# Optimization experiments

Measured on AMD Instinct MI355X. Metric: run time of the kernel, lower is better.

Reference implementation:

```python
import jax, jax.numpy as jnp
import numpy as np

NUM_NODES = 200000   # visited nodes in the temporal-KG subgraph
D = 64               # n_dims_in == n_dims_out
Q = 128              # number of query subgraphs (edges[:,0])
E = 1024             # edges per query group (equal-size groups)
NE = Q * E
RATIO = 0.0          # ratio_update
NEG_SLOPE = 0.01     # LeakyReLU default


def setup_inputs() -> dict:
    key = jax.random.key(0)
    ks = jax.random.split(key, 10)
    qid = jnp.repeat(jnp.arange(Q, dtype=jnp.int32), E)          # edges[:,0]
    src = jax.random.randint(ks[0], (NE,), 0, NUM_NODES, dtype=jnp.int32)
    dst = jax.random.randint(ks[1], (NE,), 0, NUM_NODES, dtype=jnp.int32)
    zeros = jnp.zeros((NE,), dtype=jnp.int32)
    # cols: 0=query idx, 1..5 unused metadata, 6=src (-2), 7=dst (-1)
    edges = jnp.stack([qid, zeros, zeros, zeros, zeros, zeros, src, dst], axis=1)
    std_g3 = np.sqrt(2.0 / (4 * D)).astype(np.float32)
    return {
        "node_score": jax.random.uniform(ks[2], (NUM_NODES,), dtype=jnp.float32),
        "node_repr": jax.random.normal(ks[3], (NUM_NODES, D), dtype=jnp.float32),
        "rel_emb": jax.random.normal(ks[4], (NE, D), dtype=jnp.float32),
        "query_src_ts_emb": jax.random.normal(ks[5], (Q, D), dtype=jnp.float32),
        "query_rel_emb": jax.random.normal(ks[6], (Q, D), dtype=jnp.float32),
        "Wq": jax.random.normal(ks[7], (4 * D, 4 * D), dtype=jnp.float32) * std_g3,
        "Wk": jax.random.normal(ks[8], (4 * D, 4 * D), dtype=jnp.float32) * std_g3,
        "W_lin": jax.random.normal(ks[9], (D, D), dtype=jnp.float32) * np.sqrt(2.0 / (2 * D)).astype(np.float32),
        "b_lin": jnp.zeros((D,), dtype=jnp.float32),
        "edges": edges,
        "max_edges": 128,
    }


def _segment_softmax(logits, seg, num_segments):
    # numerically stable softmax within segments (per src node)
    m = jax.ops.segment_max(logits, seg, num_segments=num_segments)
    ex = jnp.exp(logits - m[seg])
    s = jax.ops.segment_sum(ex, seg, num_segments=num_segments)
    return ex / s[seg]


def reference(node_score, node_repr, rel_emb, query_src_ts_emb, query_rel_emb,
              Wq, Wk, W_lin, b_lin, edges, max_edges):
    q = edges[:, 0]
    src = edges[:, 6]   # edges[:, -2]
    dst = edges[:, 7]   # edges[:, -1] (same as col 7 used for sparse rows)
    qs = query_src_ts_emb[q]   # [NE, D]
    qr = query_rel_emb[q]      # [NE, D]
    # G3 bilinear attention: sum(Q(left) * K(right), -1)
    left = jnp.concatenate([node_repr[src], rel_emb, qs, qr], axis=-1)   # [NE, 4D]
    right = jnp.concatenate([node_repr[dst], rel_emb, qs, qr], axis=-1)  # [NE, 4D]
    logits = jnp.sum((left @ Wq.T) * (right @ Wk.T), axis=-1)            # [NE]
    # segment softmax over src nodes, score propagation
    soft = _segment_softmax(logits, src, NUM_NODES)
    src_score = node_score[src]
    target_score = soft * src_score
    # top-k per query group (equal-size groups -> vectorized top_k)
    _, idx = jax.lax.top_k(target_score.reshape(Q, E), max_edges)        # [Q, k]
    flat = (jnp.arange(Q, dtype=idx.dtype)[:, None] * E + idx).reshape(-1)
    p_soft = soft[flat]
    p_src = src[flat]
    p_dst = dst[flat]
    p_src_score = src_score[flat]
    # sparse scatter: updated_node_score[dst] += softmax * src_score
    updated_node_score = jax.ops.segment_sum(p_soft * p_src_score, p_dst, num_segments=NUM_NODES)
    # representation update: rows src aggregate dst reprs weighted by softmax;
    # untouched nodes keep identity, touched src nodes keep ratio_update of self
    agg = jax.ops.segment_sum((1.0 - RATIO) * p_soft[:, None] * node_repr[p_dst],
                              p_src, num_segments=NUM_NODES)             # [N, D]
    is_src = jnp.zeros((NUM_NODES,), bool).at[p_src].set(True)
    diag = jnp.where(is_src, RATIO, 1.0)
    updated_repr = agg + diag[:, None] * node_repr
    # bypass_forward: LeakyReLU(Linear(.))
    out_repr = jax.nn.leaky_relu(updated_repr @ W_lin + b_lin, NEG_SLOPE)
    return updated_node_score, out_repr
```

## Files before the change

### kernel.cpp

```cpp
#include <hip/hip_runtime.h>

#define NNODES 200000
#define NQ     128
#define EPQ    1024
#define NE     (NQ*EPQ)
#define TOPK   128
#define NSEL   (NQ*TOPK)

__device__ __forceinline__ unsigned fkey(float f) {
  unsigned u = __float_as_uint(f);
  return (u & 0x80000000u) ? ~u : (u | 0x80000000u);
}
__device__ __forceinline__ float fdecode(unsigned k) {
  unsigned u = (k & 0x80000000u) ? (k ^ 0x80000000u) : ~k;
  return __uint_as_float(u);
}
__device__ __forceinline__ void fmarow(float* a, float x, const float4 n0, const float4 n1) {
  a[0] = fmaf(x, n0.x, a[0]); a[1] = fmaf(x, n0.y, a[1]);
  a[2] = fmaf(x, n0.z, a[2]); a[3] = fmaf(x, n0.w, a[3]);
  a[4] = fmaf(x, n1.x, a[4]); a[5] = fmaf(x, n1.y, a[5]);
  a[6] = fmaf(x, n1.z, a[6]); a[7] = fmaf(x, n1.w, a[7]);
}

typedef const __attribute__((address_space(1))) void* gas_ptr;
typedef __attribute__((address_space(3))) void* las_ptr;
__device__ __forceinline__ void gload16(const void* g, void* l) {
  __builtin_amdgcn_global_load_lds((gas_ptr)g, (las_ptr)l, 16, 0, 0);
}

__device__ __forceinline__ int nperm(int k) {
  const int q = k >> 2, p = k & 3;
  return (q & 1) * 64 + (q >> 1) * 4 + p;
}

__global__ __launch_bounds__(256) void k_init(unsigned* __restrict__ segmax,
                                              float* __restrict__ segsum,
                                              int* __restrict__ flag,
                                              float* __restrict__ outs) {
  const int i = blockIdx.x * 256 + threadIdx.x;
  if (i < NNODES) { segmax[i] = 0u; segsum[i] = 0.f; flag[i] = 0; outs[i] = 0.f; }
}

__global__ __launch_bounds__(256) void k_nmat(const float* __restrict__ Wq,
                                              const float* __restrict__ Wk,
                                              float* __restrict__ Nm) {
  __shared__ float ph[128];
  const int j = blockIdx.x;
  const int k = threadIdx.x & 127;
  const int ih = threadIdx.x >> 7;
  const int i0 = ih * 128;
  float a0 = 0.f, a1 = 0.f, a2 = 0.f, a3 = 0.f;
  for (int i = i0; i < i0 + 128; i += 4) {
    a0 = fmaf(Wq[(i + 0) * 256 + j], Wk[(i + 0) * 256 + k], a0);
    a1 = fmaf(Wq[(i + 1) * 256 + j], Wk[(i + 1) * 256 + k], a1);
    a2 = fmaf(Wq[(i + 2) * 256 + j], Wk[(i + 2) * 256 + k], a2);
    a3 = fmaf(Wq[(i + 3) * 256 + j], Wk[(i + 3) * 256 + k], a3);
  }
  const float p = (a0 + a1) + (a2 + a3);
  if (ih == 0) ph[k] = p;
  __syncthreads();
  if (ih == 1) Nm[j * 128 + nperm(k)] = ph[k] + p;
}

__global__ __launch_bounds__(256) void k_query(const float* __restrict__ Wq,
                                               const float* __restrict__ Wk,
                                               const float* __restrict__ qs_emb,
                                               const float* __restrict__ qr_emb,
                                               float* __restrict__ alpha,
                                               float* __restrict__ beta,
                                               float* __restrict__ cv) {
  __shared__ float sq[128];
  __shared__ float u[256], v[256];
  const int q = blockIdx.x, t = threadIdx.x;
  if (t < 64) sq[t] = qs_emb[q * 64 + t];
  else if (t < 128) sq[t] = qr_emb[q * 64 + (t - 64)];
  __syncthreads();
  {
    const float4* wq4 = (const float4*)(Wq + t * 256 + 128);
    const float4* wk4 = (const float4*)(Wk + t * 256 + 128);
    const float4* sq4 = (const float4*)sq;
    float uu = 0.f, vv = 0.f;
#pragma unroll 8
    for (int j = 0; j < 32; ++j) {
      const float4 a = wq4[j], b = wk4[j], s = sq4[j];
      uu = fmaf(a.x, s.x, fmaf(a.y, s.y, fmaf(a.z, s.z, fmaf(a.w, s.w, uu))));
      vv = fmaf(b.x, s.x, fmaf(b.y, s.y, fmaf(b.z, s.z, fmaf(b.w, s.w, vv))));
    }
    u[t] = uu; v[t] = vv;
  }
  __syncthreads();
  if (t < 128) {
    float a0 = 0.f, a1 = 0.f, a2 = 0.f, a3 = 0.f;
    for (int i = 0; i < 256; i += 4) {
      a0 = fmaf(Wq[(i + 0) * 256 + t], v[i + 0], a0);
      a1 = fmaf(Wq[(i + 1) * 256 + t], v[i + 1], a1);
      a2 = fmaf(Wq[(i + 2) * 256 + t], v[i + 2], a2);
      a3 = fmaf(Wq[(i + 3) * 256 + t], v[i + 3], a3);
    }
    alpha[q * 128 + t] = (a0 + a1) + (a2 + a3);
  } else {
    const int k = t - 128;
    float b0 = 0.f, b1 = 0.f, b2 = 0.f, b3 = 0.f;
    for (int i = 0; i < 256; i += 4) {
      b0 = fmaf(u[i + 0], Wk[(i + 0) * 256 + k], b0);
      b1 = fmaf(u[i + 1], Wk[(i + 1) * 256 + k], b1);
      b2 = fmaf(u[i + 2], Wk[(i + 2) * 256 + k], b2);
      b3 = fmaf(u[i + 3], Wk[(i + 3) * 256 + k], b3);
    }
    beta[q * 128 + k] = (b0 + b1) + (b2 + b3);
  }
  __syncthreads();
  if (t < 64) {
    float c = u[t] * v[t] + u[t + 64] * v[t + 64] + u[t + 128] * v[t + 128] + u[t + 192] * v[t + 192];
    c += __shfl_xor(c, 32, 64);
    c += __shfl_xor(c, 16, 64);
    c += __shfl_xor(c, 8, 64);
    c += __shfl_xor(c, 4, 64);
    c += __shfl_xor(c, 2, 64);
    c += __shfl_xor(c, 1, 64);
    if (t == 0) cv[q] = c;
  }
}

__global__ __launch_bounds__(512, 1) void k_logits(
    const float* __restrict__ repr, const float* __restrict__ rel,
    const int* __restrict__ edges, const float* __restrict__ Nm,
    const float* __restrict__ alpha, const float* __restrict__ beta,
    const float* __restrict__ cv, float* __restrict__ logits) {
  __shared__ float Nl[128 * 128];
  __shared__ float Xe[256 * 64];
  __shared__ float sA[128], sB[128];
  __shared__ int sSrc[256], sDst[256];
  const int t = threadIdx.x;
  const int e0 = blockIdx.x * 256;
  const int q = e0 >> 10;

  {
    const char* g = (const char*)Nm + (size_t)t * 16;
    char* l = (char*)Nl + (size_t)t * 16;
#pragma unroll
    for (int r = 0; r < 8; ++r) gload16(g + r * 8192, l + r * 8192);
  }

  if (t < 256) {
    sSrc[t] = edges[(size_t)(e0 + t) * 8 + 6];
    sDst[t] = edges[(size_t)(e0 + t) * 8 + 7];
  } else if (t < 384) {
    sA[t - 256] = alpha[q * 128 + (t - 256)];
  } else {
    sB[t - 384] = beta[q * 128 + (t - 384)];
  }

  const int elr = t >> 4, c = t & 15;
  const int swzst = (elr >> 3) & 3;
#pragma unroll
  for (int r = 0; r < 8; ++r) {
    const int el = r * 32 + elr;
    const int src = edges[(size_t)(e0 + el) * 8 + 6];
    const int cg = c ^ swzst;
    gload16((const char*)repr + ((size_t)src * 64 + cg * 4) * 4,
            (char*)Xe + ((size_t)el * 64 + c * 4) * 4);
  }
  __syncthreads();

  const int kg = t & 15, eg = t >> 4;
  const int k0 = kg * 8, eb = eg * 8;
  const int kf = kg * 4;
  const int swz = eg & 3;
  float acc[8][8];
#pragma unroll
  for (int i = 0; i < 8; ++i)
#pragma unroll
    for (int m = 0; m < 8; ++m) acc[i][m] = 0.f;

#pragma unroll 2
  for (int J = 0; J < 16; ++J) {
    const float* __restrict__ Nr = Nl + (4 * J) * 128;
    float4 n0[4], n1[4];
#pragma unroll
    for (int jj = 0; jj < 4; ++jj) {
      n0[jj] = *(const float4*)(Nr + jj * 128 + kf);
      n1[jj] = *(const float4*)(Nr + jj * 128 + 64 + kf);
    }
    const int ch = (J ^ swz) * 4;
    float4 xv[8];
#pragma unroll
    for (int i = 0; i < 8; ++i)
      xv[i] = *(const float4*)(Xe + (eb + i) * 64 + ch);
#pragma unroll
    for (int jj = 0; jj < 4; ++jj) {
#pragma unroll
      for (int i = 0; i < 8; ++i) {
        const float xs = jj == 0 ? xv[i].x : jj == 1 ? xv[i].y : jj == 2 ? xv[i].z : xv[i].w;
        fmarow(acc[i], xs, n0[jj], n1[jj]);
      }
    }
  }
  __syncthreads();

#pragma unroll
  for (int r = 0; r < 8; ++r) {
    const int el = r * 32 + elr;
    const int cg = c ^ swzst;
    gload16((const char*)rel + ((size_t)(e0 + el) * 64 + cg * 4) * 4,
            (char*)Xe + ((size_t)el * 64 + c * 4) * 4);
  }
  __syncthreads();

#pragma unroll 2
  for (int J = 0; J < 16; ++J) {
    const float* __restrict__ Nr = Nl + (64 + 4 * J) * 128;
    float4 n0[4], n1[4];
#pragma unroll
    for (int jj = 0; jj < 4; ++jj) {
      n0[jj] = *(const float4*)(Nr + jj * 128 + kf);
      n1[jj] = *(const float4*)(Nr + jj * 128 + 64 + kf);
    }
    const int ch = (J ^ swz) * 4;
    float4 xv[8];
#pragma unroll
    for (int i = 0; i < 8; ++i)
      xv[i] = *(const float4*)(Xe + (eb + i) * 64 + ch);
#pragma unroll
    for (int jj = 0; jj < 4; ++jj) {
#pragma unroll
      for (int i = 0; i < 8; ++i) {
        const float xs = jj == 0 ? xv[i].x : jj == 1 ? xv[i].y : jj == 2 ? xv[i].z : xv[i].w;
        fmarow(acc[i], xs, n0[jj], n1[jj]);
      }
    }
  }

  float aA[8], aB[8];
#pragma unroll
  for (int m = 0; m < 8; ++m) { aA[m] = sA[k0 + m]; aB[m] = sB[k0 + m]; }

  float part[8];
#pragma unroll
  for (int i = 0; i < 8; ++i) {
    const int el = eb + i;
    const int e = e0 + el;
    const float* xp;
    const float* yp;
    if (k0 < 64) {
      xp = repr + (size_t)sSrc[el] * 64 + k0;
      yp = repr + (size_t)sDst[el] * 64 + k0;
    } else {
      xp = rel + (size_t)e * 64 + (k0 - 64);
      yp = xp;
    }
    const float4 x0 = *(const float4*)xp;
    const float4 x1 = *(const float4*)(xp + 4);
    const float4 y0 = *(const float4*)yp;
    const float4 y1 = *(const float4*)(yp + 4);
    const float xs[8] = {x0.x, x0.y, x0.z, x0.w, x1.x, x1.y, x1.z, x1.w};
    const float ys[8] = {y0.x, y0.y, y0.z, y0.w, y1.x, y1.y, y1.z, y1.w};
    float p = 0.f;
#pragma unroll
    for (int m = 0; m < 8; ++m)
      p += (acc[i][m] + aB[m]) * ys[m] + aA[m] * xs[m];
    part[i] = p;
  }
#pragma unroll
  for (int i = 0; i < 8; ++i) {
    float p = part[i];
    p += __shfl_xor(p, 8, 64);
    p += __shfl_xor(p, 4, 64);
    p += __shfl_xor(p, 2, 64);
    p += __shfl_xor(p, 1, 64);
    part[i] = p;
  }
  if (kg == 0) {
    const float cq = cv[q];
    float4 o0 = {part[0] + cq, part[1] + cq, part[2] + cq, part[3] + cq};
    float4 o1 = {part[4] + cq, part[5] + cq, part[6] + cq, part[7] + cq};
    *(float4*)(logits + e0 + eb) = o0;
    *(float4*)(logits + e0 + eb + 4) = o1;
  }
}

__global__ __launch_bounds__(256) void k_segmax(const float* __restrict__ logits,
                                                const int* __restrict__ edges,
                                                unsigned* __restrict__ segmax) {
  const int e = blockIdx.x * 256 + threadIdx.x;
  const int src = edges[(size_t)e * 8 + 6];
  atomicMax(&segmax[src], fkey(logits[e]));
}

__global__ __launch_bounds__(256) void k_exsum(float* __restrict__ logits,
                                               const int* __restrict__ edges,
                                               const unsigned* __restrict__ segmax,
                                               float* __restrict__ segsum) {
  const int e = blockIdx.x * 256 + threadIdx.x;
  const int src = edges[(size_t)e * 8 + 6];
  const float m = fdecode(segmax[src]);
  const float ex = expf(logits[e] - m);
  logits[e] = ex;
  atomicAdd(&segsum[src], ex);
}

__global__ __launch_bounds__(256) void k_topk(const float* __restrict__ ex,
                                              const float* __restrict__ segsum,
                                              const int* __restrict__ edges,
                                              const float* __restrict__ node_score,
                                              int* __restrict__ sel,
                                              int* __restrict__ flag,
                                              float* __restrict__ out_score,
                                              float* agg) {
  __shared__ unsigned keys[1024];
  __shared__ int hist[256];
  __shared__ int selEl[128];
  __shared__ int eqIdx[32];
  __shared__ int sB0, sRank, sCnt, sEq;
  const int q = blockIdx.x, t = threadIdx.x;
  for (int i = t; i < 1024; i += 256) {
    const int e = q * 1024 + i;
    const int src = edges[(size_t)e * 8 + 6];
    const float ts = (ex[e] / segsum[src]) * node_score[src];
    keys[i] = fkey(ts);
  }
  unsigned prefix = 0, pmask = 0;
  int rank = 128;
  __syncthreads();
#pragma unroll
  for (int pass = 0; pass < 4; ++pass) {
    const int shift = 24 - 8 * pass;
    hist[t] = 0;
    __syncthreads();
    for (int i = t; i < 1024; i += 256) {
      const unsigned k = keys[i];
      if ((k & pmask) == prefix) atomicAdd(&hist[(k >> shift) & 255], 1);
    }
    __syncthreads();
    if (t < 64) {
      const int h0 = hist[4 * t], h1 = hist[4 * t + 1], h2 = hist[4 * t + 2], h3 = hist[4 * t + 3];
      const int s4 = h0 + h1 + h2 + h3;
      int S = s4;
      for (int d = 1; d < 64; d <<= 1) {
        const int o = __shfl_down(S, d, 64);
        if (t + d < 64) S += o;
      }
      const int Snext = S - s4;
      if (S >= rank && Snext < rank) {
        int r = rank - Snext;
        int b;
        if (r <= h3) b = 3;
        else if (r <= h3 + h2) { b = 2; r -= h3; }
        else if (r <= h3 + h2 + h1) { b = 1; r -= h3 + h2; }
        else { b = 0; r -= h3 + h2 + h1; }
        sB0 = 4 * t + b; sRank = r;
      }
    }
    __syncthreads();
    prefix |= ((unsigned)sB0) << shift;
    pmask |= 0xFFu << shift;
    rank = sRank;
    __syncthreads();
  }
  const unsigned thr = prefix;
  if (t == 0) { sCnt = 0; sEq = 0; }
  __syncthreads();
  for (int i = t; i < 1024; i += 256) {
    const unsigned k = keys[i];
    if (k > thr) { const int s = atomicAdd(&sCnt, 1); selEl[s] = i; }
    else if (k == thr) { const int j = atomicAdd(&sEq, 1); if (j < 32) eqIdx[j] = i; }
  }
  __syncthreads();
  if (t == 0) {
    int n = sEq; if (n > 32) n = 32;
    for (int a = 1; a < n; ++a) {
      const int v2 = eqIdx[a]; int b = a - 1;
      while (b >= 0 && eqIdx[b] > v2) { eqIdx[b + 1] = eqIdx[b]; --b; }
      eqIdx[b + 1] = v2;
    }
    for (int r2 = 0; r2 < rank; ++r2) selEl[sCnt + r2] = eqIdx[r2];
  }
  __syncthreads();
  if (t < 128) {
    const int el = selEl[t];
    const int e = q * 1024 + el;
    sel[q * 128 + t] = e;
    const int src = edges[(size_t)e * 8 + 6];
    const int dst = edges[(size_t)e * 8 + 7];
    const float soft = ex[e] / segsum[src];
    atomicAdd(&out_score[dst], soft * node_score[src]);
    flag[src] = 1;
  }
  __syncthreads();
  for (int i = t; i < 128 * 64; i += 256) {
    const int s = i >> 6, d = i & 63;
    const int e = q * 1024 + selEl[s];
    const int src = edges[(size_t)e * 8 + 6];
    agg[(size_t)src * 64 + d] = 0.f;
  }
}

__global__ __launch_bounds__(256) void k_scatter(const int* __restrict__ sel,
                                                 const int* __restrict__ edges,
                                                 const float* __restrict__ ex,
                                                 const float* __restrict__ segsum,
                                                 const float* __restrict__ repr,
                                                 float* agg) {
  const int i = blockIdx.x * 4 + (threadIdx.x >> 6);
  const int d = threadIdx.x & 63;
  const int e = sel[i];
  const int src = edges[(size_t)e * 8 + 6];
  const int dst = edges[(size_t)e * 8 + 7];
  const float soft = ex[e] / segsum[src];
  atomicAdd(&agg[(size_t)src * 64 + d], soft * repr[(size_t)dst * 64 + d]);
}

#define FN 192
__global__ __launch_bounds__(192) void k_final(const float* __restrict__ repr,
                                               const float* agg,
                                               const int* __restrict__ flag,
                                               const float* __restrict__ Wl,
                                               const float* __restrict__ bl,
                                               float* outr) {
  __shared__ float Ut[64][FN];
  __shared__ float W[64][64];
  __shared__ float bs[64];
  const int t = threadIdx.x;
  const int n0blk = blockIdx.x * FN;
  for (int i = t; i < 4096; i += FN) W[i >> 6][i & 63] = Wl[i];
  if (t < 64) bs[t] = bl[t];
  {
    const int n = n0blk + t;
    const bool ok = n < NNODES;
    const float* rowp = repr;
    if (ok) rowp = (flag[n] ? agg : repr) + (size_t)n * 64;
#pragma unroll
    for (int i = 0; i < 16; ++i) {
      float4 v4 = ok ? ((const float4*)rowp)[i] : float4{0.f, 0.f, 0.f, 0.f};
      const int c = i * 4;
      Ut[c + 0][t] = v4.x; Ut[c + 1][t] = v4.y; Ut[c + 2][t] = v4.z; Ut[c + 3][t] = v4.w;
    }
  }
  __syncthreads();
  const int dg = t & 7, ng = t >> 3;
  const int d0 = dg * 8, nb = ng * 8;
  float acc[8][8];
#pragma unroll
  for (int i = 0; i < 8; ++i)
#pragma unroll
    for (int m = 0; m < 8; ++m) acc[i][m] = 0.f;
#pragma unroll 2
  for (int c = 0; c < 64; ++c) {
    const float4 w0 = *(const float4*)&W[c][d0];
    const float4 w1 = *(const float4*)&W[c][d0 + 4];
    const float4 u0 = *(const float4*)&Ut[c][nb];
    const float4 u1 = *(const float4*)&Ut[c][nb + 4];
    fmarow(acc[0], u0.x, w0, w1);
    fmarow(acc[1], u0.y, w0, w1);
    fmarow(acc[2], u0.z, w0, w1);
    fmarow(acc[3], u0.w, w0, w1);
    fmarow(acc[4], u1.x, w0, w1);
    fmarow(acc[5], u1.y, w0, w1);
    fmarow(acc[6], u1.z, w0, w1);
    fmarow(acc[7], u1.w, w0, w1);
  }
  float bb[8];
#pragma unroll
  for (int m = 0; m < 8; ++m) bb[m] = bs[d0 + m];
#pragma unroll
  for (int i = 0; i < 8; ++i) {
    const int n = n0blk + nb + i;
    if (n < NNODES) {
      float o[8];
#pragma unroll
      for (int m = 0; m < 8; ++m) {
        float v = acc[i][m] + bb[m];
        o[m] = v > 0.f ? v : 0.01f * v;
      }
      float4 o0 = {o[0], o[1], o[2], o[3]};
      float4 o1 = {o[4], o[5], o[6], o[7]};
      *(float4*)(outr + (size_t)n * 64 + d0) = o0;
      *(float4*)(outr + (size_t)n * 64 + d0 + 4) = o1;
    }
  }
}

extern "C" void kernel_launch(void* const* d_in, const int* in_sizes, int n_in,
                              void* d_out, int out_size, void* d_ws, size_t ws_size,
                              hipStream_t stream) {
  const float* node_score = (const float*)d_in[0];
  const float* node_repr  = (const float*)d_in[1];
  const float* rel_emb    = (const float*)d_in[2];
  const float* qs_emb     = (const float*)d_in[3];
  const float* qr_emb     = (const float*)d_in[4];
  const float* Wq         = (const float*)d_in[5];
  const float* Wk         = (const float*)d_in[6];
  const float* Wl         = (const float*)d_in[7];
  const float* bl         = (const float*)d_in[8];
  const int*   edges      = (const int*)d_in[9];

  float* out_score = (float*)d_out;
  float* out_repr  = out_score + NNODES;

  float* ws = (float*)d_ws;
  size_t o = 0;
  float* Nm      = ws + o; o += 128 * 128;
  float* alpha   = ws + o; o += NQ * 128;
  float* beta    = ws + o; o += NQ * 128;
  float* cv      = ws + o; o += NQ;
  float* exl     = ws + o; o += NE;
  unsigned* segmax = (unsigned*)(ws + o); o += NNODES;
  float* segsum  = ws + o; o += NNODES;
  int* sel       = (int*)(ws + o); o += NSEL;
  int* flag      = (int*)(ws + o); o += NNODES;

  k_init<<<(NNODES + 255) / 256, 256, 0, stream>>>(segmax, segsum, flag, out_score);
  k_nmat<<<128, 256, 0, stream>>>(Wq, Wk, Nm);
  k_query<<<NQ, 256, 0, stream>>>(Wq, Wk, qs_emb, qr_emb, alpha, beta, cv);
  k_logits<<<NE / 256, 512, 0, stream>>>(node_repr, rel_emb, edges, Nm, alpha, beta, cv, exl);
  k_segmax<<<NE / 256, 256, 0, stream>>>(exl, edges, segmax);
  k_exsum<<<NE / 256, 256, 0, stream>>>(exl, edges, segmax, segsum);
  k_topk<<<NQ, 256, 0, stream>>>(exl, segsum, edges, node_score, sel, flag, out_score, out_repr);
  k_scatter<<<NSEL / 4, 256, 0, stream>>>(sel, edges, exl, segsum, node_repr, out_repr);
  k_final<<<(NNODES + FN - 1) / FN, FN, 0, stream>>>(node_repr, out_repr, flag, Wl, bl, out_repr);
}
```

Baseline: 175.6 us.

## Double-buffer edge feature chunks and double edges per block in logits kernel

The logits kernel now processes 512 edges per block instead of 256, with each thread accumulating 16 edges. The 128-wide input features (gathered repr then rel) are streamed in 16-column chunks through a two-slot LDS buffer, so the next chunk's async load overlaps the current chunk's FMAs. This halves how often the 64KB N matrix is loaded per edge and hides gather latency. In exchange the grid shrinks to 256 blocks, there are more syncs, and register pressure roughly doubles with 128 accumulators per thread, which risks spills.

```diff
diff --git a/kernel.cpp b/kernel.cpp
--- a/kernel.cpp
+++ b/kernel.cpp
@@ -128,11 +128,11 @@
     const float* __restrict__ alpha, const float* __restrict__ beta,
     const float* __restrict__ cv, float* __restrict__ logits) {
   __shared__ float Nl[128 * 128];
-  __shared__ float Xe[256 * 64];
+  __shared__ float Xp[2][512 * 16];
   __shared__ float sA[128], sB[128];
-  __shared__ int sSrc[256], sDst[256];
+  __shared__ int sSrc[512], sDst[512];
   const int t = threadIdx.x;
-  const int e0 = blockIdx.x * 256;
+  const int e0 = blockIdx.x * 512;
   const int q = e0 >> 10;
 
   {
@@ -142,102 +142,89 @@
     for (int r = 0; r < 8; ++r) gload16(g + r * 8192, l + r * 8192);
   }
 
-  if (t < 256) {
-    sSrc[t] = edges[(size_t)(e0 + t) * 8 + 6];
-    sDst[t] = edges[(size_t)(e0 + t) * 8 + 7];
-  } else if (t < 384) {
-    sA[t - 256] = alpha[q * 128 + (t - 256)];
-  } else {
-    sB[t - 384] = beta[q * 128 + (t - 384)];
-  }
-
-  const int elr = t >> 4, c = t & 15;
-  const int swzst = (elr >> 3) & 3;
-#pragma unroll
-  for (int r = 0; r < 8; ++r) {
-    const int el = r * 32 + elr;
+  {
+    const size_t e = (size_t)(e0 + t);
+    sSrc[t] = edges[e * 8 + 6];
+    sDst[t] = edges[e * 8 + 7];
+    if (t < 128) sA[t] = alpha[q * 128 + t];
+    else if (t < 256) sB[t - 128] = beta[q * 128 + (t - 128)];
+  }
+
+  const int elr = t >> 2, cc = t & 3;
+#pragma unroll
+  for (int r = 0; r < 4; ++r) {
+    const int el = r * 128 + elr;
     const int src = edges[(size_t)(e0 + el) * 8 + 6];
-    const int cg = c ^ swzst;
+    const int cg = cc ^ ((el >> 4) & 3);
     gload16((const char*)repr + ((size_t)src * 64 + cg * 4) * 4,
-            (char*)Xe + ((size_t)el * 64 + c * 4) * 4);
+            (char*)&Xp[0][0] + (size_t)r * 8192 + (size_t)t * 16);
   }
   __syncthreads();
 
   const int kg = t & 15, eg = t >> 4;
-  const int k0 = kg * 8, eb = eg * 8;
+  const int k0 = kg * 8, eb = eg * 16;
   const int kf = kg * 4;
   const int swz = eg & 3;
-  float acc[8][8];
-#pragma unroll
-  for (int i = 0; i < 8; ++i)
+  float acc[16][8];
+#pragma unroll
+  for (int i = 0; i < 16; ++i)
 #pragma unroll
     for (int m = 0; m < 8; ++m) acc[i][m] = 0.f;
 
-#pragma unroll 2
-  for (int J = 0; J < 16; ++J) {
-    const float* __restrict__ Nr = Nl + (4 * J) * 128;
-    float4 n0[4], n1[4];
-#pragma unroll
-    for (int jj = 0; jj < 4; ++jj) {
-      n0[jj] = *(const float4*)(Nr + jj * 128 + kf);
-      n1[jj] = *(const float4*)(Nr + jj * 128 + 64 + kf);
-    }
-    const int ch = (J ^ swz) * 4;
-    float4 xv[8];
-#pragma unroll
-    for (int i = 0; i < 8; ++i)
-      xv[i] = *(const float4*)(Xe + (eb + i) * 64 + ch);
-#pragma unroll
-    for (int jj = 0; jj < 4; ++jj) {
-#pragma unroll
-      for (int i = 0; i < 8; ++i) {
-        const float xs = jj == 0 ? xv[i].x : jj == 1 ? xv[i].y : jj == 2 ? xv[i].z : xv[i].w;
-        fmarow(acc[i], xs, n0[jj], n1[jj]);
+  for (int p = 0; p < 8; ++p) {
+    if (p < 7) {
+      const int pn = p + 1;
+      char* ldst = (char*)&Xp[pn & 1][0] + (size_t)t * 16;
+      if (pn < 4) {
+#pragma unroll
+        for (int r = 0; r < 4; ++r) {
+          const int el = r * 128 + elr;
+          const int src = sSrc[el];
+          const int cg = cc ^ ((el >> 4) & 3);
+          gload16((const char*)repr + ((size_t)src * 64 + pn * 16 + cg * 4) * 4,
+                  ldst + r * 8192);
+        }
+      } else {
+#pragma unroll
+        for (int r = 0; r < 4; ++r) {
+          const int el = r * 128 + elr;
+          const int cg = cc ^ ((el >> 4) & 3);
+          gload16((const char*)rel + ((size_t)(e0 + el) * 64 + (pn - 4) * 16 + cg * 4) * 4,
+                  ldst + r * 8192);
+        }
       }
     }
-  }
-  __syncthreads();
-
-#pragma unroll
-  for (int r = 0; r < 8; ++r) {
-    const int el = r * 32 + elr;
-    const int cg = c ^ swzst;
-    gload16((const char*)rel + ((size_t)(e0 + el) * 64 + cg * 4) * 4,
-            (char*)Xe + ((size_t)el * 64 + c * 4) * 4);
-  }
-  __syncthreads();
-
-#pragma unroll 2
-  for (int J = 0; J < 16; ++J) {
-    const float* __restrict__ Nr = Nl + (64 + 4 * J) * 128;
-    float4 n0[4], n1[4];
-#pragma unroll
-    for (int jj = 0; jj < 4; ++jj) {
-      n0[jj] = *(const float4*)(Nr + jj * 128 + kf);
-      n1[jj] = *(const float4*)(Nr + jj * 128 + 64 + kf);
-    }
-    const int ch = (J ^ swz) * 4;
-    float4 xv[8];
-#pragma unroll
-    for (int i = 0; i < 8; ++i)
-      xv[i] = *(const float4*)(Xe + (eb + i) * 64 + ch);
-#pragma unroll
-    for (int jj = 0; jj < 4; ++jj) {
-#pragma unroll
-      for (int i = 0; i < 8; ++i) {
-        const float xs = jj == 0 ? xv[i].x : jj == 1 ? xv[i].y : jj == 2 ? xv[i].z : xv[i].w;
-        fmarow(acc[i], xs, n0[jj], n1[jj]);
+    const float* __restrict__ Xb = &Xp[p & 1][0];
+#pragma unroll
+    for (int J = 0; J < 4; ++J) {
+      const int jb = p * 16 + J * 4;
+      float4 n0[4], n1[4];
+#pragma unroll
+      for (int jj = 0; jj < 4; ++jj) {
+        const float* Nr = Nl + (jb + jj) * 128;
+        n0[jj] = *(const float4*)(Nr + kf);
+        n1[jj] = *(const float4*)(Nr + 64 + kf);
       }
-    }
+      const int ch = (J ^ swz) * 4;
+#pragma unroll
+      for (int i = 0; i < 16; ++i) {
+        const float4 xv = *(const float4*)(Xb + (eb + i) * 16 + ch);
+        fmarow(acc[i], xv.x, n0[0], n1[0]);
+        fmarow(acc[i], xv.y, n0[1], n1[1]);
+        fmarow(acc[i], xv.z, n0[2], n1[2]);
+        fmarow(acc[i], xv.w, n0[3], n1[3]);
+      }
+    }
+    __syncthreads();
   }
 
   float aA[8], aB[8];
 #pragma unroll
   for (int m = 0; m < 8; ++m) { aA[m] = sA[k0 + m]; aB[m] = sB[k0 + m]; }
 
-  float part[8];
-#pragma unroll
-  for (int i = 0; i < 8; ++i) {
+  float part[16];
+#pragma unroll
+  for (int i = 0; i < 16; ++i) {
     const int el = eb + i;
     const int e = e0 + el;
     const float* xp;
@@ -262,7 +249,7 @@
     part[i] = p;
   }
 #pragma unroll
-  for (int i = 0; i < 8; ++i) {
+  for (int i = 0; i < 16; ++i) {
     float p = part[i];
     p += __shfl_xor(p, 8, 64);
     p += __shfl_xor(p, 4, 64);
@@ -272,10 +259,12 @@
   }
   if (kg == 0) {
     const float cq = cv[q];
-    float4 o0 = {part[0] + cq, part[1] + cq, part[2] + cq, part[3] + cq};
-    float4 o1 = {part[4] + cq, part[5] + cq, part[6] + cq, part[7] + cq};
-    *(float4*)(logits + e0 + eb) = o0;
-    *(float4*)(logits + e0 + eb + 4) = o1;
+#pragma unroll
+    for (int w = 0; w < 4; ++w) {
+      float4 o = {part[w * 4 + 0] + cq, part[w * 4 + 1] + cq,
+                  part[w * 4 + 2] + cq, part[w * 4 + 3] + cq};
+      *(float4*)(logits + e0 + eb + w * 4) = o;
+    }
   }
 }
 
@@ -512,7 +501,7 @@
   k_init<<<(NNODES + 255) / 256, 256, 0, stream>>>(segmax, segsum, flag, out_score);
   k_nmat<<<128, 256, 0, stream>>>(Wq, Wk, Nm);
   k_query<<<NQ, 256, 0, stream>>>(Wq, Wk, qs_emb, qr_emb, alpha, beta, cv);
-  k_logits<<<NE / 256, 512, 0, stream>>>(node_repr, rel_emb, edges, Nm, alpha, beta, cv, exl);
+  k_logits<<<NE / 512, 512, 0, stream>>>(node_repr, rel_emb, edges, Nm, alpha, beta, cv, exl);
   k_segmax<<<NE / 256, 256, 0, stream>>>(exl, edges, segmax);
   k_exsum<<<NE / 256, 256, 0, stream>>>(exl, edges, segmax, segsum);
   k_topk<<<NQ, 256, 0, stream>>>(exl, segsum, edges, node_score, sel, flag, out_score, out_repr);
```

New measurement: 252.7 us. 43.9% more time.

## Merge setup kernels, fuse segment-max into logits, compact edge src/dst columns

Applied to the files above, without the earlier changes.

Folds the init, N-matrix and per-query kernels into one launch that dispatches on block index. The segment-max atomics move into the logits kernel's epilogue, and the logits kernel writes compact src/dst arrays that later kernels read instead of the strided 8-int edge rows. The top-k kernel goes from 256 to 512 threads per block. This removes three launches and one pass over logits and edges, at the cost of extra workspace and more atomic traffic in the logits epilogue.

```diff
diff --git a/kernel.cpp b/kernel.cpp
--- a/kernel.cpp
+++ b/kernel.cpp
@@ -33,45 +33,43 @@
   return (q & 1) * 64 + (q >> 1) * 4 + p;
 }
 
-__global__ __launch_bounds__(256) void k_init(unsigned* __restrict__ segmax,
-                                              float* __restrict__ segsum,
-                                              int* __restrict__ flag,
-                                              float* __restrict__ outs) {
-  const int i = blockIdx.x * 256 + threadIdx.x;
-  if (i < NNODES) { segmax[i] = 0u; segsum[i] = 0.f; flag[i] = 0; outs[i] = 0.f; }
-}
-
-__global__ __launch_bounds__(256) void k_nmat(const float* __restrict__ Wq,
-                                              const float* __restrict__ Wk,
-                                              float* __restrict__ Nm) {
+#define NB_INIT 782
+
+__global__ __launch_bounds__(256) void k_setup(
+    const float* __restrict__ Wq, const float* __restrict__ Wk,
+    const float* __restrict__ qs_emb, const float* __restrict__ qr_emb,
+    unsigned* __restrict__ segmax, float* __restrict__ segsum,
+    int* __restrict__ flag, float* __restrict__ outs,
+    float* __restrict__ Nm, float* __restrict__ alpha,
+    float* __restrict__ beta, float* __restrict__ cv) {
   __shared__ float ph[128];
-  const int j = blockIdx.x;
-  const int k = threadIdx.x & 127;
-  const int ih = threadIdx.x >> 7;
-  const int i0 = ih * 128;
-  float a0 = 0.f, a1 = 0.f, a2 = 0.f, a3 = 0.f;
-  for (int i = i0; i < i0 + 128; i += 4) {
-    a0 = fmaf(Wq[(i + 0) * 256 + j], Wk[(i + 0) * 256 + k], a0);
-    a1 = fmaf(Wq[(i + 1) * 256 + j], Wk[(i + 1) * 256 + k], a1);
-    a2 = fmaf(Wq[(i + 2) * 256 + j], Wk[(i + 2) * 256 + k], a2);
-    a3 = fmaf(Wq[(i + 3) * 256 + j], Wk[(i + 3) * 256 + k], a3);
-  }
-  const float p = (a0 + a1) + (a2 + a3);
-  if (ih == 0) ph[k] = p;
-  __syncthreads();
-  if (ih == 1) Nm[j * 128 + nperm(k)] = ph[k] + p;
-}
-
-__global__ __launch_bounds__(256) void k_query(const float* __restrict__ Wq,
-                                               const float* __restrict__ Wk,
-                                               const float* __restrict__ qs_emb,
-                                               const float* __restrict__ qr_emb,
-                                               float* __restrict__ alpha,
-                                               float* __restrict__ beta,
-                                               float* __restrict__ cv) {
   __shared__ float sq[128];
   __shared__ float u[256], v[256];
-  const int q = blockIdx.x, t = threadIdx.x;
+  const int b = blockIdx.x, t = threadIdx.x;
+  if (b < NB_INIT) {
+    const int i = b * 256 + t;
+    if (i < NNODES) { segmax[i] = 0u; segsum[i] = 0.f; flag[i] = 0; outs[i] = 0.f; }
+    return;
+  }
+  if (b < NB_INIT + 128) {
+    const int j = b - NB_INIT;
+    const int k = t & 127;
+    const int ih = t >> 7;
+    const int i0 = ih * 128;
+    float a0 = 0.f, a1 = 0.f, a2 = 0.f, a3 = 0.f;
+    for (int i = i0; i < i0 + 128; i += 4) {
+      a0 = fmaf(Wq[(i + 0) * 256 + j], Wk[(i + 0) * 256 + k], a0);
+      a1 = fmaf(Wq[(i + 1) * 256 + j], Wk[(i + 1) * 256 + k], a1);
+      a2 = fmaf(Wq[(i + 2) * 256 + j], Wk[(i + 2) * 256 + k], a2);
+      a3 = fmaf(Wq[(i + 3) * 256 + j], Wk[(i + 3) * 256 + k], a3);
+    }
+    const float p = (a0 + a1) + (a2 + a3);
+    if (ih == 0) ph[k] = p;
+    __syncthreads();
+    if (ih == 1) Nm[j * 128 + nperm(k)] = ph[k] + p;
+    return;
+  }
+  const int q = b - NB_INIT - 128;
   if (t < 64) sq[t] = qs_emb[q * 64 + t];
   else if (t < 128) sq[t] = qr_emb[q * 64 + (t - 64)];
   __syncthreads();
@@ -82,9 +80,9 @@
     float uu = 0.f, vv = 0.f;
 #pragma unroll 8
     for (int j = 0; j < 32; ++j) {
-      const float4 a = wq4[j], b = wk4[j], s = sq4[j];
+      const float4 a = wq4[j], bb = wk4[j], s = sq4[j];
       uu = fmaf(a.x, s.x, fmaf(a.y, s.y, fmaf(a.z, s.z, fmaf(a.w, s.w, uu))));
-      vv = fmaf(b.x, s.x, fmaf(b.y, s.y, fmaf(b.z, s.z, fmaf(b.w, s.w, vv))));
+      vv = fmaf(bb.x, s.x, fmaf(bb.y, s.y, fmaf(bb.z, s.z, fmaf(bb.w, s.w, vv))));
     }
     u[t] = uu; v[t] = vv;
   }
@@ -126,7 +124,8 @@
     const float* __restrict__ repr, const float* __restrict__ rel,
     const int* __restrict__ edges, const float* __restrict__ Nm,
     const float* __restrict__ alpha, const float* __restrict__ beta,
-    const float* __restrict__ cv, float* __restrict__ logits) {
+    const float* __restrict__ cv, float* __restrict__ logits,
+    unsigned* __restrict__ segmax, int* __restrict__ csrc, int* __restrict__ cdst) {
   __shared__ float Nl[128 * 128];
   __shared__ float Xe[256 * 64];
   __shared__ float sA[128], sB[128];
@@ -143,8 +142,10 @@
   }
 
   if (t < 256) {
-    sSrc[t] = edges[(size_t)(e0 + t) * 8 + 6];
-    sDst[t] = edges[(size_t)(e0 + t) * 8 + 7];
+    const int src = edges[(size_t)(e0 + t) * 8 + 6];
+    const int dst = edges[(size_t)(e0 + t) * 8 + 7];
+    sSrc[t] = src; sDst[t] = dst;
+    csrc[e0 + t] = src; cdst[e0 + t] = dst;
   } else if (t < 384) {
     sA[t - 256] = alpha[q * 128 + (t - 256)];
   } else {
@@ -272,36 +273,35 @@
   }
   if (kg == 0) {
     const float cq = cv[q];
-    float4 o0 = {part[0] + cq, part[1] + cq, part[2] + cq, part[3] + cq};
-    float4 o1 = {part[4] + cq, part[5] + cq, part[6] + cq, part[7] + cq};
+    float lo[8];
+#pragma unroll
+    for (int i = 0; i < 8; ++i) lo[i] = part[i] + cq;
+    float4 o0 = {lo[0], lo[1], lo[2], lo[3]};
+    float4 o1 = {lo[4], lo[5], lo[6], lo[7]};
     *(float4*)(logits + e0 + eb) = o0;
     *(float4*)(logits + e0 + eb + 4) = o1;
-  }
-}
-
-__global__ __launch_bounds__(256) void k_segmax(const float* __restrict__ logits,
-                                                const int* __restrict__ edges,
-                                                unsigned* __restrict__ segmax) {
-  const int e = blockIdx.x * 256 + threadIdx.x;
-  const int src = edges[(size_t)e * 8 + 6];
-  atomicMax(&segmax[src], fkey(logits[e]));
+#pragma unroll
+    for (int i = 0; i < 8; ++i)
+      atomicMax(&segmax[sSrc[eb + i]], fkey(lo[i]));
+  }
 }
 
 __global__ __launch_bounds__(256) void k_exsum(float* __restrict__ logits,
-                                               const int* __restrict__ edges,
+                                               const int* __restrict__ csrc,
                                                const unsigned* __restrict__ segmax,
                                                float* __restrict__ segsum) {
   const int e = blockIdx.x * 256 + threadIdx.x;
-  const int src = edges[(size_t)e * 8 + 6];
+  const int src = csrc[e];
   const float m = fdecode(segmax[src]);
   const float ex = expf(logits[e] - m);
   logits[e] = ex;
   atomicAdd(&segsum[src], ex);
 }
 
-__global__ __launch_bounds__(256) void k_topk(const float* __restrict__ ex,
+__global__ __launch_bounds__(512) void k_topk(const float* __restrict__ ex,
                                               const float* __restrict__ segsum,
-                                              const int* __restrict__ edges,
+                                              const int* __restrict__ csrc,
+                                              const int* __restrict__ cdst,
                                               const float* __restrict__ node_score,
                                               int* __restrict__ sel,
                                               int* __restrict__ flag,
@@ -313,9 +313,9 @@
   __shared__ int eqIdx[32];
   __shared__ int sB0, sRank, sCnt, sEq;
   const int q = blockIdx.x, t = threadIdx.x;
-  for (int i = t; i < 1024; i += 256) {
+  for (int i = t; i < 1024; i += 512) {
     const int e = q * 1024 + i;
-    const int src = edges[(size_t)e * 8 + 6];
+    const int src = csrc[e];
     const float ts = (ex[e] / segsum[src]) * node_score[src];
     keys[i] = fkey(ts);
   }
@@ -325,9 +325,9 @@
 #pragma unroll
   for (int pass = 0; pass < 4; ++pass) {
     const int shift = 24 - 8 * pass;
-    hist[t] = 0;
+    if (t < 256) hist[t] = 0;
     __syncthreads();
-    for (int i = t; i < 1024; i += 256) {
+    for (int i = t; i < 1024; i += 512) {
       const unsigned k = keys[i];
       if ((k & pmask) == prefix) atomicAdd(&hist[(k >> shift) & 255], 1);
     }
@@ -360,7 +360,7 @@
   const unsigned thr = prefix;
   if (t == 0) { sCnt = 0; sEq = 0; }
   __syncthreads();
-  for (int i = t; i < 1024; i += 256) {
+  for (int i = t; i < 1024; i += 512) {
     const unsigned k = keys[i];
     if (k > thr) { const int s = atomicAdd(&sCnt, 1); selEl[s] = i; }
     else if (k == thr) { const int j = atomicAdd(&sEq, 1); if (j < 32) eqIdx[j] = i; }
@@ -380,23 +380,24 @@
     const int el = selEl[t];
     const int e = q * 1024 + el;
     sel[q * 128 + t] = e;
-    const int src = edges[(size_t)e * 8 + 6];
-    const int dst = edges[(size_t)e * 8 + 7];
+    const int src = csrc[e];
+    const int dst = cdst[e];
     const float soft = ex[e] / segsum[src];
     atomicAdd(&out_score[dst], soft * node_score[src]);
     flag[src] = 1;
   }
   __syncthreads();
-  for (int i = t; i < 128 * 64; i += 256) {
+  for (int i = t; i < 128 * 64; i += 512) {
     const int s = i >> 6, d = i & 63;
     const int e = q * 1024 + selEl[s];
-    const int src = edges[(size_t)e * 8 + 6];
+    const int src = csrc[e];
     agg[(size_t)src * 64 + d] = 0.f;
   }
 }
 
 __global__ __launch_bounds__(256) void k_scatter(const int* __restrict__ sel,
-                                                 const int* __restrict__ edges,
+                                                 const int* __restrict__ csrc,
+                                                 const int* __restrict__ cdst,
                                                  const float* __restrict__ ex,
                                                  const float* __restrict__ segsum,
                                                  const float* __restrict__ repr,
@@ -404,8 +405,8 @@
   const int i = blockIdx.x * 4 + (threadIdx.x >> 6);
   const int d = threadIdx.x & 63;
   const int e = sel[i];
-  const int src = edges[(size_t)e * 8 + 6];
-  const int dst = edges[(size_t)e * 8 + 7];
+  const int src = csrc[e];
+  const int dst = cdst[e];
   const float soft = ex[e] / segsum[src];
   atomicAdd(&agg[(size_t)src * 64 + d], soft * repr[(size_t)dst * 64 + d]);
 }
@@ -508,14 +509,19 @@
   float* segsum  = ws + o; o += NNODES;
   int* sel       = (int*)(ws + o); o += NSEL;
   int* flag      = (int*)(ws + o); o += NNODES;
-
-  k_init<<<(NNODES + 255) / 256, 256, 0, stream>>>(segmax, segsum, flag, out_score);
-  k_nmat<<<128, 256, 0, stream>>>(Wq, Wk, Nm);
-  k_query<<<NQ, 256, 0, stream>>>(Wq, Wk, qs_emb, qr_emb, alpha, beta, cv);
-  k_logits<<<NE / 256, 512, 0, stream>>>(node_repr, rel_emb, edges, Nm, alpha, beta, cv, exl);
-  k_segmax<<<NE / 256, 256, 0, stream>>>(exl, edges, segmax);
-  k_exsum<<<NE / 256, 256, 0, stream>>>(exl, edges, segmax, segsum);
-  k_topk<<<NQ, 256, 0, stream>>>(exl, segsum, edges, node_score, sel, flag, out_score, out_repr);
-  k_scatter<<<NSEL / 4, 256, 0, stream>>>(sel, edges, exl, segsum, node_repr, out_repr);
-  k_final<<<(NNODES + FN - 1) / FN, FN, 0, stream>>>(node_repr, out_repr, flag, Wl, bl, out_repr);
-}
+  int* csrc      = (int*)(ws + o); o += NE;
+  int* cdst      = (int*)(ws + o); o += NE;
+
+  k_setup<<<NB_INIT + 256, 256, 0, stream>>>(Wq, Wk, qs_emb, qr_emb,
+                                             segmax, segsum, flag, out_score,
+                                             Nm, alpha, beta, cv);
+  k_logits<<<NE / 256, 512, 0, stream>>>(node_repr, rel_emb, edges, Nm, alpha,
+                                         beta, cv, exl, segmax, csrc, cdst);
+  k_exsum<<<NE / 256, 256, 0, stream>>>(exl, csrc, segmax, segsum);
+  k_topk<<<NQ, 512, 0, stream>>>(exl, segsum, csrc, cdst, node_score, sel, flag,
+                                 out_score, out_repr);
+  k_scatter<<<NSEL / 4, 256, 0, stream>>>(sel, csrc, cdst, exl, segsum,
+                                          node_repr, out_repr);
+  k_final<<<(NNODES + FN - 1) / FN, FN, 0, stream>>>(node_repr, out_repr, flag,
+                                                     Wl, bl, out_repr);
+}
```

Result: faster. 155.7 us (-11.4%).
